# Optimization experiments

Hardware: AMD Instinct MI355X
Metric: run time of the kernel (lower is better)

## Reference

```python
import jax, jax.numpy as jnp
import numpy as np

VOCAB, D = 5, 64


def setup_inputs() -> dict:
    key = jax.random.key(0)
    ks = jax.random.split(key, 8)
    B, S = 8, 2048
    x = jax.random.randint(ks[0], (B, S), 0, VOCAB)
    emb_table = jax.random.normal(ks[1], (VOCAB, D), dtype=jnp.float32)
    wq = jax.random.normal(ks[2], (D, D), dtype=jnp.float32) * 0.1
    bq = jax.random.normal(ks[3], (D,), dtype=jnp.float32) * 0.1
    wk = jax.random.normal(ks[4], (D, D), dtype=jnp.float32) * 0.1
    bk = jax.random.normal(ks[5], (D,), dtype=jnp.float32) * 0.1
    wv = jax.random.normal(ks[6], (D, D), dtype=jnp.float32) * 0.1
    bv = jax.random.normal(ks[7], (D,), dtype=jnp.float32) * 0.1
    return {"x": x, "emb_table": emb_table, "wq": wq, "bq": bq,
            "wk": wk, "bk": bk, "wv": wv, "bv": bv}


def reference(x, emb_table, wq, bq, wk, bk, wv, bv):
    # Embedding lookup: [B, S, D]
    emb = emb_table[x]
    # torch Linear: y = x @ W.T + b
    Q = emb @ wq.T + bq
    K = emb @ wk.T + bk
    V = emb @ wv.T + bv
    scale = 1.0 / np.sqrt(D).astype(np.float32)
    # [B, S, S] attention scores
    scores = jnp.einsum('bqd,bkd->bqk', Q, K) * scale
    S_len = x.shape[-1]
    # causal mask: -inf strictly above the diagonal
    causal = jnp.tril(jnp.ones((S_len, S_len), dtype=bool))
    scores = jnp.where(causal, scores, jnp.float32(-jnp.inf))
    probs = jax.nn.softmax(scores, axis=-1)
    return jnp.einsum('bqk,bkd->bqd', probs, V)
```

## Files before the change

### kernel.cpp

```cpp
#include <hip/hip_runtime.h>
#include <math.h>

#define VOCAB 5
#define DIM   64
#define BATCH 8
#define SLEN  2048
#define SEG   64
#define SEGS_PER_B (SLEN / SEG)
#define BLOCK 512
#define WPAD  65

__global__ __launch_bounds__(BLOCK) void decoder_fused(
    const int* __restrict__ x, const float* __restrict__ emb,
    const float* __restrict__ wq, const float* __restrict__ bq,
    const float* __restrict__ wk, const float* __restrict__ bk,
    const float* __restrict__ wv, const float* __restrict__ bv,
    float* __restrict__ out)
{
    const int bid  = blockIdx.x;
    const int b    = bid >> 5;
    const int seg  = bid & 31;
    const int s0   = seg * SEG;
    const int t    = threadIdx.x;
    const int lane = t & 63;
    const int wave = t >> 6;

    __shared__ float wSh[3][DIM * WPAD];
    __shared__ float eSh[VOCAB * DIM];
    __shared__ float qSh[VOCAB * WPAD];
    __shared__ float kSh[VOCAB * WPAD];
    __shared__ __align__(16) float vSh[VOCAB * DIM];
    __shared__ float StabSh[VOCAB * VOCAB];
    __shared__ float pSh[SEG * VOCAB];
    __shared__ int   wcSh[4][VOCAB];

    const int* xb = x + b * SLEN;

    int tok = 0;
    int inc[VOCAB] = {0, 0, 0, 0, 0};

    if (wave < 4) {
        const float4* wq4 = (const float4*)wq;
        const float4* wk4 = (const float4*)wk;
        const float4* wv4 = (const float4*)wv;
        for (int j = t; j < DIM * DIM / 4; j += 256) {
            int d = j >> 4, i4 = (j & 15) << 2;
            float4 a = wq4[j];
            float* dst = &wSh[0][d * WPAD + i4];
            dst[0] = a.x; dst[1] = a.y; dst[2] = a.z; dst[3] = a.w;
        }
        for (int j = t; j < DIM * DIM / 4; j += 256) {
            int d = j >> 4, i4 = (j & 15) << 2;
            float4 a = wk4[j];
            float* dst = &wSh[1][d * WPAD + i4];
            dst[0] = a.x; dst[1] = a.y; dst[2] = a.z; dst[3] = a.w;
        }
        for (int j = t; j < DIM * DIM / 4; j += 256) {
            int d = j >> 4, i4 = (j & 15) << 2;
            float4 a = wv4[j];
            float* dst = &wSh[2][d * WPAD + i4];
            dst[0] = a.x; dst[1] = a.y; dst[2] = a.z; dst[3] = a.w;
        }
    } else {
        for (int i = t - 256; i < VOCAB * DIM; i += 256) eSh[i] = emb[i];

        const int pw = wave - 4;
        int base[VOCAB] = {0, 0, 0, 0, 0};
        const int nchunk = s0 >> 6;
        for (int c = pw; c < nchunk; c += 4) {
            int tk = xb[(c << 6) + lane];
            #pragma unroll
            for (int v = 0; v < VOCAB; ++v)
                base[v] += __popcll(__ballot(tk == v));
        }
        if (lane == 0) {
            #pragma unroll
            for (int v = 0; v < VOCAB; ++v) wcSh[pw][v] = base[v];
        }
        if (wave == 7) {
            tok = xb[s0 + lane];
            const unsigned long long leMask = (2ull << lane) - 1ull;
            #pragma unroll
            for (int v = 0; v < VOCAB; ++v)
                inc[v] = __popcll(__ballot(tok == v) & leMask);
        }
    }
    __syncthreads();

    if (wave < 5) {
        const int v = wave, d = lane;
        float aq = bq[d], ak = bk[d], av = bv[d];
        const float* e  = &eSh[v * DIM];
        const float* rq = &wSh[0][d * WPAD];
        const float* rk = &wSh[1][d * WPAD];
        const float* rv = &wSh[2][d * WPAD];
        #pragma unroll 16
        for (int i = 0; i < DIM; ++i) {
            float ei = e[i];
            aq += ei * rq[i];
            ak += ei * rk[i];
            av += ei * rv[i];
        }
        qSh[v * WPAD + d] = aq;
        kSh[v * WPAD + d] = ak;
        vSh[v * DIM + d]  = av;
    }
    __syncthreads();

    if (t < VOCAB * VOCAB) {
        int i = t / VOCAB, j = t % VOCAB;
        float s = 0.f;
        #pragma unroll 16
        for (int d = 0; d < DIM; ++d)
            s += qSh[i * WPAD + d] * kSh[j * WPAD + d];
        StabSh[t] = s * 0.125f;
    }
    __syncthreads();

    if (wave == 7) {
        float sv[VOCAB];
        #pragma unroll
        for (int v = 0; v < VOCAB; ++v) sv[v] = StabSh[tok * VOCAB + v];
        float mx = fmaxf(fmaxf(fmaxf(sv[0], sv[1]), fmaxf(sv[2], sv[3])), sv[4]);
        float wgt[VOCAB];
        float den = 0.f;
        #pragma unroll
        for (int v = 0; v < VOCAB; ++v) {
            int c = inc[v] + wcSh[0][v] + wcSh[1][v] + wcSh[2][v] + wcSh[3][v];
            float wv = (float)c * expf(sv[v] - mx);
            wgt[v] = wv;
            den += wv;
        }
        float invd = 1.0f / den;
        #pragma unroll
        for (int v = 0; v < VOCAB; ++v) pSh[lane * VOCAB + v] = wgt[v] * invd;
    }
    __syncthreads();

    const float4* Vs4 = reinterpret_cast<const float4*>(vSh);
    float4* out4 = reinterpret_cast<float4*>(out) + ((size_t)b * SLEN + s0) * (DIM / 4);
    for (int i = t; i < SEG * (DIM / 4); i += BLOCK) {
        int q = i >> 4, d4 = i & 15;
        float4 acc = make_float4(0.f, 0.f, 0.f, 0.f);
        #pragma unroll
        for (int v = 0; v < VOCAB; ++v) {
            float pw = pSh[q * VOCAB + v];
            float4 vv = Vs4[v * (DIM / 4) + d4];
            acc.x += pw * vv.x;
            acc.y += pw * vv.y;
            acc.z += pw * vv.z;
            acc.w += pw * vv.w;
        }
        out4[i] = acc;
    }
}

extern "C" void kernel_launch(void* const* d_in, const int* in_sizes, int n_in,
                              void* d_out, int out_size, void* d_ws, size_t ws_size,
                              hipStream_t stream) {
    const int*   x   = (const int*)d_in[0];
    const float* emb = (const float*)d_in[1];
    const float* wq  = (const float*)d_in[2];
    const float* bq  = (const float*)d_in[3];
    const float* wk  = (const float*)d_in[4];
    const float* bk  = (const float*)d_in[5];
    const float* wv  = (const float*)d_in[6];
    const float* bv  = (const float*)d_in[7];
    float* out = (float*)d_out;

    decoder_fused<<<BATCH * SEGS_PER_B, BLOCK, 0, stream>>>(
        x, emb, wq, bq, wk, bk, wv, bv, out);
}
```

Measured before the change: 11.11 us.

## Fuse softmax weights into output loop, vectorize token counting, batch weight loads

Removes the separate softmax phase and its barrier by having every thread recompute the per-query softmax weights inline in the output loop, using token and count tables staged in shared memory. Prefix token counting now uses int4 loads with per-lane counts and shuffle reductions across three waves instead of per-chunk ballots across four. All weight float4 loads are issued before any shared-memory stores, and bias loads are hoisted ahead of the first barrier to overlap global latency. In exchange, exp work is duplicated 16x per query and more shared memory is used.

```diff
diff --git a/kernel.cpp b/kernel.cpp
--- a/kernel.cpp
+++ b/kernel.cpp
@@ -31,65 +31,72 @@
     __shared__ float kSh[VOCAB * WPAD];
     __shared__ __align__(16) float vSh[VOCAB * DIM];
     __shared__ float StabSh[VOCAB * VOCAB];
-    __shared__ float pSh[SEG * VOCAB];
-    __shared__ int   wcSh[4][VOCAB];
+    __shared__ int   tokSh[SEG];
+    __shared__ int   incSh[SEG][VOCAB];
+    __shared__ float cntFSh[SEG][VOCAB];
+    __shared__ int   wcSh[3][VOCAB];
 
     const int* xb = x + b * SLEN;
 
-    int tok = 0;
-    int inc[VOCAB] = {0, 0, 0, 0, 0};
+    float aq = 0.f, ak = 0.f, av = 0.f;
+    if (wave < 5) { aq = bq[lane]; ak = bk[lane]; av = bv[lane]; }
 
     if (wave < 4) {
         const float4* wq4 = (const float4*)wq;
         const float4* wk4 = (const float4*)wk;
         const float4* wv4 = (const float4*)wv;
-        for (int j = t; j < DIM * DIM / 4; j += 256) {
-            int d = j >> 4, i4 = (j & 15) << 2;
-            float4 a = wq4[j];
-            float* dst = &wSh[0][d * WPAD + i4];
-            dst[0] = a.x; dst[1] = a.y; dst[2] = a.z; dst[3] = a.w;
+        float4 rq[4], rk[4], rv[4];
+        #pragma unroll
+        for (int it = 0; it < 4; ++it) {
+            rq[it] = wq4[t + 256 * it];
+            rk[it] = wk4[t + 256 * it];
+            rv[it] = wv4[t + 256 * it];
         }
-        for (int j = t; j < DIM * DIM / 4; j += 256) {
-            int d = j >> 4, i4 = (j & 15) << 2;
-            float4 a = wk4[j];
-            float* dst = &wSh[1][d * WPAD + i4];
-            dst[0] = a.x; dst[1] = a.y; dst[2] = a.z; dst[3] = a.w;
-        }
-        for (int j = t; j < DIM * DIM / 4; j += 256) {
-            int d = j >> 4, i4 = (j & 15) << 2;
-            float4 a = wv4[j];
-            float* dst = &wSh[2][d * WPAD + i4];
-            dst[0] = a.x; dst[1] = a.y; dst[2] = a.z; dst[3] = a.w;
+        #pragma unroll
+        for (int it = 0; it < 4; ++it) {
+            int j = t + 256 * it, d = j >> 4, i4 = (j & 15) << 2;
+            float* dq = &wSh[0][d * WPAD + i4];
+            float* dk = &wSh[1][d * WPAD + i4];
+            float* dv = &wSh[2][d * WPAD + i4];
+            dq[0]=rq[it].x; dq[1]=rq[it].y; dq[2]=rq[it].z; dq[3]=rq[it].w;
+            dk[0]=rk[it].x; dk[1]=rk[it].y; dk[2]=rk[it].z; dk[3]=rk[it].w;
+            dv[0]=rv[it].x; dv[1]=rv[it].y; dv[2]=rv[it].z; dv[3]=rv[it].w;
         }
     } else {
         for (int i = t - 256; i < VOCAB * DIM; i += 256) eSh[i] = emb[i];
 
-        const int pw = wave - 4;
-        int base[VOCAB] = {0, 0, 0, 0, 0};
-        const int nchunk = s0 >> 6;
-        for (int c = pw; c < nchunk; c += 4) {
-            int tk = xb[(c << 6) + lane];
+        if (wave < 7) {
+            const int pw = wave - 4;
+            const int n4 = s0 >> 2;
+            const int4* xb4 = (const int4*)xb;
+            int c[VOCAB] = {0,0,0,0,0};
+            for (int idx = pw * 64 + lane; idx < n4; idx += 192) {
+                int4 tk = xb4[idx];
+                #pragma unroll
+                for (int v = 0; v < VOCAB; ++v)
+                    c[v] += (tk.x==v) + (tk.y==v) + (tk.z==v) + (tk.w==v);
+            }
             #pragma unroll
-            for (int v = 0; v < VOCAB; ++v)
-                base[v] += __popcll(__ballot(tk == v));
-        }
-        if (lane == 0) {
-            #pragma unroll
-            for (int v = 0; v < VOCAB; ++v) wcSh[pw][v] = base[v];
-        }
-        if (wave == 7) {
-            tok = xb[s0 + lane];
+            for (int v = 0; v < VOCAB; ++v) {
+                int s = c[v];
+                #pragma unroll
+                for (int off = 32; off > 0; off >>= 1)
+                    s += __shfl_xor(s, off, 64);
+                if (lane == 0) wcSh[pw][v] = s;
+            }
+        } else {
+            int tok = xb[s0 + lane];
+            tokSh[lane] = tok;
             const unsigned long long leMask = (2ull << lane) - 1ull;
             #pragma unroll
             for (int v = 0; v < VOCAB; ++v)
-                inc[v] = __popcll(__ballot(tok == v) & leMask);
+                incSh[lane][v] = __popcll(__ballot(tok == v) & leMask);
         }
     }
     __syncthreads();
 
     if (wave < 5) {
         const int v = wave, d = lane;
-        float aq = bq[d], ak = bk[d], av = bv[d];
         const float* e  = &eSh[v * DIM];
         const float* rq = &wSh[0][d * WPAD];
         const float* rk = &wSh[1][d * WPAD];
@@ -104,6 +111,11 @@
         qSh[v * WPAD + d] = aq;
         kSh[v * WPAD + d] = ak;
         vSh[v * DIM + d]  = av;
+    } else if (wave == 5) {
+        #pragma unroll
+        for (int v = 0; v < VOCAB; ++v)
+            cntFSh[lane][v] = (float)(incSh[lane][v]
+                               + wcSh[0][v] + wcSh[1][v] + wcSh[2][v]);
     }
     __syncthreads();
 
@@ -117,34 +129,30 @@
     }
     __syncthreads();
 
-    if (wave == 7) {
-        float sv[VOCAB];
+    const float4* Vs4 = reinterpret_cast<const float4*>(vSh);
+    float4* out4 = reinterpret_cast<float4*>(out) + ((size_t)b * SLEN + s0) * (DIM / 4);
+    #pragma unroll
+    for (int it = 0; it < 2; ++it) {
+        const int i  = t + BLOCK * it;
+        const int q  = i >> 4;
+        const int d4 = i & 15;
+        const int tok = tokSh[q];
+        float sv[VOCAB], wgt[VOCAB];
         #pragma unroll
         for (int v = 0; v < VOCAB; ++v) sv[v] = StabSh[tok * VOCAB + v];
         float mx = fmaxf(fmaxf(fmaxf(sv[0], sv[1]), fmaxf(sv[2], sv[3])), sv[4]);
-        float wgt[VOCAB];
         float den = 0.f;
         #pragma unroll
         for (int v = 0; v < VOCAB; ++v) {
-            int c = inc[v] + wcSh[0][v] + wcSh[1][v] + wcSh[2][v] + wcSh[3][v];
-            float wv = (float)c * expf(sv[v] - mx);
+            float wv = cntFSh[q][v] * expf(sv[v] - mx);
             wgt[v] = wv;
             den += wv;
         }
-        float invd = 1.0f / den;
-        #pragma unroll
-        for (int v = 0; v < VOCAB; ++v) pSh[lane * VOCAB + v] = wgt[v] * invd;
-    }
-    __syncthreads();
-
-    const float4* Vs4 = reinterpret_cast<const float4*>(vSh);
-    float4* out4 = reinterpret_cast<float4*>(out) + ((size_t)b * SLEN + s0) * (DIM / 4);
-    for (int i = t; i < SEG * (DIM / 4); i += BLOCK) {
-        int q = i >> 4, d4 = i & 15;
+        const float inv = 1.0f / den;
         float4 acc = make_float4(0.f, 0.f, 0.f, 0.f);
         #pragma unroll
         for (int v = 0; v < VOCAB; ++v) {
-            float pw = pSh[q * VOCAB + v];
+            float pw = wgt[v] * inv;
             float4 vv = Vs4[v * (DIM / 4) + d4];
             acc.x += pw * vv.x;
             acc.y += pw * vv.y;
```

Result: slower. 12.56 us (+13.1%).

## Fold softmax weights into output loop and drop a barrier stage

Applied to the files above, without the earlier changes.

Moves token loading and inclusive counts into shared memory. The exponentiated 5x5 score table is now computed by the score threads. Per-query weights are recomputed redundantly in the output loop, so the separate softmax stage and one __syncthreads are gone. Prefix counting now uses three waves instead of four, and bias loads are hoisted before the first barrier. Dropping the max subtraction risks overflow for large scores, and the redundant per-thread weight computation adds ALU and LDS reads.

```diff
diff --git a/kernel.cpp b/kernel.cpp
--- a/kernel.cpp
+++ b/kernel.cpp
@@ -30,14 +30,16 @@
     __shared__ float qSh[VOCAB * WPAD];
     __shared__ float kSh[VOCAB * WPAD];
     __shared__ __align__(16) float vSh[VOCAB * DIM];
-    __shared__ float StabSh[VOCAB * VOCAB];
-    __shared__ float pSh[SEG * VOCAB];
-    __shared__ int   wcSh[4][VOCAB];
+    __shared__ float ESh[VOCAB * VOCAB];
+    __shared__ int   tokSh[SEG];
+    __shared__ int   incSh[SEG][VOCAB];
+    __shared__ float cntFSh[SEG][VOCAB];
+    __shared__ int   wcSh[3][VOCAB];
 
     const int* xb = x + b * SLEN;
 
-    int tok = 0;
-    int inc[VOCAB] = {0, 0, 0, 0, 0};
+    float aq = 0.f, ak = 0.f, av = 0.f;
+    if (wave < 5) { aq = bq[lane]; ak = bk[lane]; av = bv[lane]; }
 
     if (wave < 4) {
         const float4* wq4 = (const float4*)wq;
@@ -64,32 +66,33 @@
     } else {
         for (int i = t - 256; i < VOCAB * DIM; i += 256) eSh[i] = emb[i];
 
-        const int pw = wave - 4;
-        int base[VOCAB] = {0, 0, 0, 0, 0};
-        const int nchunk = s0 >> 6;
-        for (int c = pw; c < nchunk; c += 4) {
-            int tk = xb[(c << 6) + lane];
-            #pragma unroll
-            for (int v = 0; v < VOCAB; ++v)
-                base[v] += __popcll(__ballot(tk == v));
-        }
-        if (lane == 0) {
-            #pragma unroll
-            for (int v = 0; v < VOCAB; ++v) wcSh[pw][v] = base[v];
-        }
-        if (wave == 7) {
-            tok = xb[s0 + lane];
+        if (wave < 7) {
+            const int pw = wave - 4;
+            int base[VOCAB] = {0, 0, 0, 0, 0};
+            const int nchunk = s0 >> 6;
+            for (int c = pw; c < nchunk; c += 3) {
+                int tk = xb[(c << 6) + lane];
+                #pragma unroll
+                for (int v = 0; v < VOCAB; ++v)
+                    base[v] += __popcll(__ballot(tk == v));
+            }
+            if (lane == 0) {
+                #pragma unroll
+                for (int v = 0; v < VOCAB; ++v) wcSh[pw][v] = base[v];
+            }
+        } else {
+            int tok = xb[s0 + lane];
+            tokSh[lane] = tok;
             const unsigned long long leMask = (2ull << lane) - 1ull;
             #pragma unroll
             for (int v = 0; v < VOCAB; ++v)
-                inc[v] = __popcll(__ballot(tok == v) & leMask);
+                incSh[lane][v] = __popcll(__ballot(tok == v) & leMask);
         }
     }
     __syncthreads();
 
     if (wave < 5) {
         const int v = wave, d = lane;
-        float aq = bq[d], ak = bk[d], av = bv[d];
         const float* e  = &eSh[v * DIM];
         const float* rq = &wSh[0][d * WPAD];
         const float* rk = &wSh[1][d * WPAD];
@@ -104,6 +107,11 @@
         qSh[v * WPAD + d] = aq;
         kSh[v * WPAD + d] = ak;
         vSh[v * DIM + d]  = av;
+    } else if (wave == 5) {
+        #pragma unroll
+        for (int v = 0; v < VOCAB; ++v)
+            cntFSh[lane][v] = (float)(incSh[lane][v]
+                               + wcSh[0][v] + wcSh[1][v] + wcSh[2][v]);
     }
     __syncthreads();
 
@@ -113,38 +121,31 @@
         #pragma unroll 16
         for (int d = 0; d < DIM; ++d)
             s += qSh[i * WPAD + d] * kSh[j * WPAD + d];
-        StabSh[t] = s * 0.125f;
-    }
-    __syncthreads();
-
-    if (wave == 7) {
-        float sv[VOCAB];
-        #pragma unroll
-        for (int v = 0; v < VOCAB; ++v) sv[v] = StabSh[tok * VOCAB + v];
-        float mx = fmaxf(fmaxf(fmaxf(sv[0], sv[1]), fmaxf(sv[2], sv[3])), sv[4]);
-        float wgt[VOCAB];
-        float den = 0.f;
-        #pragma unroll
-        for (int v = 0; v < VOCAB; ++v) {
-            int c = inc[v] + wcSh[0][v] + wcSh[1][v] + wcSh[2][v] + wcSh[3][v];
-            float wv = (float)c * expf(sv[v] - mx);
-            wgt[v] = wv;
-            den += wv;
-        }
-        float invd = 1.0f / den;
-        #pragma unroll
-        for (int v = 0; v < VOCAB; ++v) pSh[lane * VOCAB + v] = wgt[v] * invd;
+        ESh[t] = expf(s * 0.125f);
     }
     __syncthreads();
 
     const float4* Vs4 = reinterpret_cast<const float4*>(vSh);
     float4* out4 = reinterpret_cast<float4*>(out) + ((size_t)b * SLEN + s0) * (DIM / 4);
-    for (int i = t; i < SEG * (DIM / 4); i += BLOCK) {
-        int q = i >> 4, d4 = i & 15;
+    #pragma unroll
+    for (int it = 0; it < 2; ++it) {
+        const int i  = t + BLOCK * it;
+        const int q  = i >> 4;
+        const int d4 = i & 15;
+        const int tok = tokSh[q];
+        float wgt[VOCAB];
+        float den = 0.f;
+        #pragma unroll
+        for (int v = 0; v < VOCAB; ++v) {
+            float wv = cntFSh[q][v] * ESh[tok * VOCAB + v];
+            wgt[v] = wv;
+            den += wv;
+        }
+        const float inv = 1.0f / den;
         float4 acc = make_float4(0.f, 0.f, 0.f, 0.f);
         #pragma unroll
         for (int v = 0; v < VOCAB; ++v) {
-            float pw = pSh[q * VOCAB + v];
+            float pw = wgt[v] * inv;
             float4 vv = Vs4[v * (DIM / 4) + d4];
             acc.x += pw * vv.x;
             acc.y += pw * vv.y;
```

New measurement: 11.43 us. +2.9%, slower.
